# Optimization experiments

Hardware: AMD Instinct MI355X
Metric: run time of the kernel (lower is better)

The kernel has to match this reference:

```python
import jax, jax.numpy as jnp
import numpy as np

B, I, O, G = 4096, 256, 256, 8
GRID_MIN, GRID_MAX, RHO = -2.0, 2.0, 1.0


def setup_inputs() -> dict:
    key = jax.random.key(0)
    ks = jax.random.split(key, 8)
    return {
        "x_re": jax.random.normal(ks[0], (B, I), dtype=jnp.float32),
        "x_im": jax.random.normal(ks[1], (B, I), dtype=jnp.float32),
        "realweights": jax.random.normal(ks[2], (I, O, G, G), dtype=jnp.float32),
        "complexweights": jax.random.normal(ks[3], (I, O, G, G), dtype=jnp.float32),
        "silu_weight_re": jax.random.normal(ks[4], (I, O), dtype=jnp.float32),
        "silu_weight_im": jax.random.normal(ks[5], (I, O), dtype=jnp.float32),
        "silu_bias_re": 0.1 * jax.random.normal(ks[6], (I, O), dtype=jnp.float32),
        "silu_bias_im": 0.1 * jax.random.normal(ks[7], (I, O), dtype=jnp.float32),
    }


def reference(x_re, x_im, realweights, complexweights,
              silu_weight_re, silu_weight_im, silu_bias_re, silu_bias_im):
    # Complex grid: grid[u, v] = lin[u] + i * lin[v]
    lin = jnp.linspace(GRID_MIN, GRID_MAX, G, dtype=x_re.dtype)
    # |x - grid|^2 = (x_re - lin_u)^2 + (x_im - lin_v)^2  -> (B, I, G, G)
    dre = x_re[:, :, None, None] - lin[None, None, :, None]
    dim = x_im[:, :, None, None] - lin[None, None, None, :]
    basis = jnp.exp(-(dre * dre + dim * dim) / RHO)  # real-valued (B, I, G, G)
    # RBF contraction: real and imaginary output channels
    out_re = jnp.einsum('biuv,iouv->bo', basis, realweights)
    out_im = jnp.einsum('biuv,iouv->bo', basis, complexweights)
    # Complex SiLU (complex_weight variant): silu applied component-wise,
    # then complex-multiplied by silu_weight, plus bias, summed over i.
    s_re = jax.nn.silu(x_re)  # (B, I)
    s_im = jax.nn.silu(x_im)
    out_re = out_re + s_re @ silu_weight_re - s_im @ silu_weight_im + jnp.sum(silu_bias_re, axis=0)
    out_im = out_im + s_im @ silu_weight_re + s_re @ silu_weight_im + jnp.sum(silu_bias_im, axis=0)
    # Return complex output as stacked (real, imag): (B, O, 2)
    return jnp.stack([out_re, out_im], axis=-1)
```

## Files before the change

kernel.cpp:

```cpp
#include <hip/hip_runtime.h>
#include <hip/hip_fp16.h>
#include <stdint.h>

typedef float floatx4 __attribute__((ext_vector_type(4)));
typedef short short8 __attribute__((ext_vector_type(8)));

constexpr int I_SZ = 256, O_SZ = 256, NCOL = 512, B_SZ = 4096;
constexpr int KSTEPS = 264;
constexpr float GSTEP = 4.0f / 7.0f;
constexpr float NLOG2E = -1.44269504088896f;

__device__ __forceinline__ uint32_t pk_bf16(float lo, float hi) {
  return __builtin_amdgcn_perm(__float_as_uint(hi), __float_as_uint(lo), 0x07060302u);
}
__device__ __forceinline__ short rne_bf16(float f) {
  uint32_t u = __float_as_uint(f);
  return (short)((u + 0x7FFFu + ((u >> 16) & 1u)) >> 16);
}

__device__ __forceinline__ void gload_lds16(const void* g, void* l) {
  __builtin_amdgcn_global_load_lds((const __attribute__((address_space(1))) void*)g,
                                   (__attribute__((address_space(3))) void*)l,
                                   16, 0, 0);
}

__device__ __forceinline__ float silu_f(float a) {
  return a * __builtin_amdgcn_rcpf(1.f + __builtin_amdgcn_exp2f(a * NLOG2E));
}

__global__ void pack_weights(const float* __restrict__ rw, const float* __restrict__ cw,
                             const float* __restrict__ swre, const float* __restrict__ swim,
                             short* __restrict__ wpack) {
  int idx = blockIdx.x * 256 + threadIdx.x;
  int n = idx & 511;
  int slot = (idx >> 9) & 3;
  int ph = (idx >> 11) & 1;
  int s = idx >> 12;
  int u = ph * 4 + slot;
  int o = n >> 1, c = n & 1;
  float w[8];
  if (s < 256) {
    const float* W = (c ? cw : rw) + (((size_t)s * O_SZ + o) << 6) + (u << 3);
    float4 a = *(const float4*)W;
    float4 b = *(const float4*)(W + 4);
    w[0] = a.x; w[1] = a.y; w[2] = a.z; w[3] = a.w;
    w[4] = b.x; w[5] = b.y; w[6] = b.z; w[7] = b.w;
  } else {
    int kp0 = ((s - 256) << 6) + (u << 3);
    #pragma unroll
    for (int e = 0; e < 8; ++e) {
      int kp = kp0 + e, i = kp >> 1, ci = kp & 1;
      float a = swre[i * O_SZ + o], b = swim[i * O_SZ + o];
      w[e] = (c == 0) ? (ci == 0 ? a : -b) : (ci == 0 ? b : a);
    }
  }
  uint32_t h[8];
  #pragma unroll
  for (int e = 0; e < 8; ++e) h[e] = (uint32_t)(uint16_t)rne_bf16(w[e]);
  uint4 val = make_uint4(h[0] | (h[1] << 16), h[2] | (h[3] << 16),
                         h[4] | (h[5] << 16), h[6] | (h[7] << 16));
  *(uint4*)(wpack + (size_t)idx * 8) = val;
}

__global__ void transpose_x(const float* __restrict__ xre, const float* __restrict__ xim,
                            __half* __restrict__ xT) {
  __shared__ float tile[64][65];
  int bt = blockIdx.x & 63;
  int it = (blockIdx.x >> 6) & 3;
  int c  = blockIdx.x >> 8;
  const float* src = (c ? xim : xre);
  int b0 = bt << 6, i0 = it << 6;
  int t = threadIdx.x;
  int il = t & 63, bh = t >> 6;
  #pragma unroll
  for (int k = 0; k < 16; ++k) {
    int bl = bh + (k << 2);
    tile[bl][il] = src[(size_t)(b0 + bl) * I_SZ + i0 + il];
  }
  __syncthreads();
  int bl2 = t & 63, ih = t >> 6;
  __half* dst = xT + ((size_t)c * I_SZ + i0) * B_SZ + b0;
  #pragma unroll
  for (int k = 0; k < 16; ++k) {
    int il2 = ih + (k << 2);
    dst[(size_t)il2 * B_SZ + bl2] = __float2half(tile[bl2][il2]);
  }
}

__global__ void bias_sums(const float* __restrict__ bre, const float* __restrict__ bim,
                          float* __restrict__ bsum) {
  int n = blockIdx.x, o = n >> 1, l = threadIdx.x;
  const float* src = ((n & 1) ? bim : bre) + o;
  float s = 0.f;
  #pragma unroll
  for (int a = 0; a < 4; ++a) s += src[(size_t)(a * 64 + l) * O_SZ];
  #pragma unroll
  for (int off = 32; off; off >>= 1) s += __shfl_down(s, off, 64);
  if (l == 0) bsum[n] = s;
}

__global__ __launch_bounds__(512, 4) void cvkan_gemm(
    const float* __restrict__ xre, const float* __restrict__ xim,
    const __half* __restrict__ xT,
    const short* __restrict__ wpack, const float* __restrict__ bsum,
    float* __restrict__ out) {
  __shared__ __align__(16) short As[4 * 128 * 8];
  __shared__ __align__(16) short Bs[2][4 * 256 * 8];

  const int tid = threadIdx.x;
  const int bid = blockIdx.x;
  const int kch = bid & 7;
  const int mn = bid >> 3;
  const int mt = mn >> 1, nt = mn & 1;
  const int b0 = mt * 128, n0 = nt * 256;
  const int l = tid & 63, w = tid >> 6;
  const int wr = w >> 2, wc = w & 3;
  const int lm = l & 15, q = l >> 4;
  const int ar = tid & 127, au = tid >> 7;

  const __half* xTre = xT;
  const __half* xTim = xT + (size_t)I_SZ * B_SZ;

  floatx4 acc[4][4] = {};
  uint4 rA;
  float eiv[8];
  float xr_s;

  auto stage_B = [&](short* bdst, int t) {
    int js = t >> 1, ph = t & 1;
    int s = (js < 32) ? (kch * 32 + js) : (256 + kch);
    const short* src = wpack + (size_t)(s * 2 + ph) * 16384 + ((tid >> 8) << 12)
                       + (n0 << 3) + ((tid & 255) << 3);
    short* ldst = bdst + (w << 9);
    gload_lds16(src,        ldst);
    gload_lds16(src + 8192, ldst + 4096);
  };

  auto build_rbf = [&](int u, float xr) {
    float d = xr - (-2.0f + u * GSTEP);
    float er = __builtin_amdgcn_exp2f(d * d * NLOG2E);
    rA = make_uint4(pk_bf16(er * eiv[0], er * eiv[1]), pk_bf16(er * eiv[2], er * eiv[3]),
                    pk_bf16(er * eiv[4], er * eiv[5]), pk_bf16(er * eiv[6], er * eiv[7]));
  };

  auto build_silu = [&](int s, int u) {
    int sl = s - 256;
    const float* pr = xre + (size_t)(b0 + ar) * I_SZ + (sl << 5) + (u << 2);
    const float* pi = xim + (size_t)(b0 + ar) * I_SZ + (sl << 5) + (u << 2);
    rA = make_uint4(pk_bf16(silu_f(pr[0]), silu_f(pi[0])),
                    pk_bf16(silu_f(pr[1]), silu_f(pi[1])),
                    pk_bf16(silu_f(pr[2]), silu_f(pi[2])),
                    pk_bf16(silu_f(pr[3]), silu_f(pi[3])));
  };

  stage_B(&Bs[0][0], 0);
  {
    int s0 = kch * 32;
    float xi0 = __half2float(xTim[(size_t)s0 * B_SZ + b0 + ar]);
    xr_s = __half2float(xTre[(size_t)s0 * B_SZ + b0 + ar]);
    #pragma unroll
    for (int v = 0; v < 8; ++v) {
      float d = xi0 - (-2.0f + v * GSTEP);
      eiv[v] = __builtin_amdgcn_exp2f(d * d * NLOG2E);
    }
    build_rbf(au, xr_s);
  }

  short* bc = &Bs[0][0];
  short* bn = &Bs[1][0];
  float xr_n = 0.f, xi_n = 0.f;

  for (int t = 0; t < 66; ++t) {
    if (t < 65 && (t & 1) == 1) {
      int jsn = (t + 1) >> 1;
      if (jsn < 32) {
        int sn = kch * 32 + jsn;
        xr_n = __half2float(xTre[(size_t)sn * B_SZ + b0 + ar]);
        xi_n = __half2float(xTim[(size_t)sn * B_SZ + b0 + ar]);
      }
    }
    __builtin_amdgcn_sched_barrier(0);

    if (t < 65) stage_B(bn, t + 1);
    *(uint4*)(As + (au << 10) + (ar << 3)) = rA;

    if (t < 65) asm volatile("s_waitcnt vmcnt(2) lgkmcnt(0)" ::: "memory");
    else        asm volatile("s_waitcnt vmcnt(0) lgkmcnt(0)" ::: "memory");
    __builtin_amdgcn_s_barrier();

    if (t < 65) {
      int tn = t + 1, jsn = tn >> 1, phn = tn & 1;
      int sn = (jsn < 32) ? (kch * 32 + jsn) : (256 + kch);
      if (sn >= 256) {
        build_silu(sn, phn * 4 + au);
      } else if (phn == 0) {
        xr_s = xr_n;
        #pragma unroll
        for (int v = 0; v < 8; ++v) {
          float d = xi_n - (-2.0f + v * GSTEP);
          eiv[v] = __builtin_amdgcn_exp2f(d * d * NLOG2E);
        }
        build_rbf(au, xr_s);
      } else {
        build_rbf(4 + au, xr_s);
      }
    }

    short8 bf[4];
    #pragma unroll
    for (int nn = 0; nn < 4; ++nn)
      bf[nn] = *(const short8*)(bc + (q << 11) + ((wc * 64 + nn * 16 + lm) << 3));
    __builtin_amdgcn_s_setprio(1);
    #pragma unroll
    for (int mm = 0; mm < 4; ++mm) {
      short8 a = *(const short8*)(As + (q << 10) + ((wr * 64 + mm * 16 + lm) << 3));
      #pragma unroll
      for (int nn = 0; nn < 4; ++nn)
        acc[mm][nn] = __builtin_amdgcn_mfma_f32_16x16x32_bf16(a, bf[nn], acc[mm][nn], 0, 0, 0);
    }
    __builtin_amdgcn_s_setprio(0);

    if (t < 65) __builtin_amdgcn_s_barrier();
    short* tmp = bc; bc = bn; bn = tmp;
  }

  #pragma unroll
  for (int nn = 0; nn < 4; ++nn) {
    int col = n0 + wc * 64 + nn * 16 + lm;
    float bv = (kch == 7) ? bsum[col] : 0.0f;
    #pragma unroll
    for (int mm = 0; mm < 4; ++mm) {
      int row0 = b0 + wr * 64 + mm * 16 + (q << 2);
      #pragma unroll
      for (int r2 = 0; r2 < 4; ++r2)
        atomicAdd(out + (size_t)(row0 + r2) * NCOL + col, acc[mm][nn][r2] + bv);
    }
  }
}

extern "C" void kernel_launch(void* const* d_in, const int* in_sizes, int n_in,
                              void* d_out, int out_size, void* d_ws, size_t ws_size,
                              hipStream_t stream) {
  const float* xre  = (const float*)d_in[0];
  const float* xim  = (const float*)d_in[1];
  const float* rw   = (const float*)d_in[2];
  const float* cw   = (const float*)d_in[3];
  const float* swre = (const float*)d_in[4];
  const float* swim = (const float*)d_in[5];
  const float* bre  = (const float*)d_in[6];
  const float* bim  = (const float*)d_in[7];
  float* out = (float*)d_out;

  size_t wpack_bytes = (size_t)KSTEPS * NCOL * 64 * 2;
  short* wpack = (short*)d_ws;
  float* bsum  = (float*)((char*)d_ws + wpack_bytes);
  __half* xT   = (__half*)((char*)d_ws + wpack_bytes + 2048);

  hipMemsetAsync(d_out, 0, (size_t)B_SZ * NCOL * sizeof(float), stream);
  pack_weights<<<(KSTEPS * NCOL * 8) / 256, 256, 0, stream>>>(rw, cw, swre, swim, wpack);
  transpose_x<<<512, 256, 0, stream>>>(xre, xim, xT);
  bias_sums<<<NCOL, 64, 0, stream>>>(bre, bim, bsum);
  cvkan_gemm<<<512, 512, 0, stream>>>(xre, xim, xT, wpack, bsum, out);
}
```

Baseline: 232.5 us.

## Shrink GEMM tile to 128x128 with 256-thread blocks and restructure pipeline

Changes the fused RBF/SiLU GEMM from 128x256 tiles with 512 threads to 128x128 tiles with 256 threads and 1024 blocks. Each thread now builds two A-slices, recomputing the imaginary exponentials every step instead of caching them across phases. The pipeline is reworked so A is built after compute, between two full barriers, with a full vmcnt(0) wait. The aim is more blocks in flight and smaller LDS per block. The cost is more redundant RBF exp work, since each A tile is now built for twice as many N-tiles, plus extra barriers and a weaker load/compute overlap.

```diff
diff --git a/kernel.cpp b/kernel.cpp
--- a/kernel.cpp
+++ b/kernel.cpp
@@ -26,6 +26,12 @@
 
 __device__ __forceinline__ float silu_f(float a) {
   return a * __builtin_amdgcn_rcpf(1.f + __builtin_amdgcn_exp2f(a * NLOG2E));
+}
+
+__device__ __forceinline__ float h2f_raw(unsigned short u) {
+  _Float16 h;
+  __builtin_memcpy(&h, &u, 2);
+  return (float)h;
 }
 
 __global__ void pack_weights(const float* __restrict__ rw, const float* __restrict__ cw,
@@ -99,129 +105,126 @@
   if (l == 0) bsum[n] = s;
 }
 
-__global__ __launch_bounds__(512, 4) void cvkan_gemm(
+__global__ __launch_bounds__(256, 4) void cvkan_gemm(
     const float* __restrict__ xre, const float* __restrict__ xim,
     const __half* __restrict__ xT,
     const short* __restrict__ wpack, const float* __restrict__ bsum,
     float* __restrict__ out) {
   __shared__ __align__(16) short As[4 * 128 * 8];
-  __shared__ __align__(16) short Bs[2][4 * 256 * 8];
+  __shared__ __align__(16) short Bs[2][4 * 128 * 8];
 
   const int tid = threadIdx.x;
   const int bid = blockIdx.x;
   const int kch = bid & 7;
   const int mn = bid >> 3;
-  const int mt = mn >> 1, nt = mn & 1;
-  const int b0 = mt * 128, n0 = nt * 256;
+  const int mt = mn >> 2, nt = mn & 3;
+  const int b0 = mt * 128, n0 = nt * 128;
   const int l = tid & 63, w = tid >> 6;
-  const int wr = w >> 2, wc = w & 3;
+  const int wr = w >> 1, wc = w & 1;
   const int lm = l & 15, q = l >> 4;
-  const int ar = tid & 127, au = tid >> 7;
+  const int r = tid >> 1, h = tid & 1;
 
   const __half* xTre = xT;
   const __half* xTim = xT + (size_t)I_SZ * B_SZ;
 
   floatx4 acc[4][4] = {};
-  uint4 rA;
-  float eiv[8];
-  float xr_s;
 
   auto stage_B = [&](short* bdst, int t) {
     int js = t >> 1, ph = t & 1;
     int s = (js < 32) ? (kch * 32 + js) : (256 + kch);
-    const short* src = wpack + (size_t)(s * 2 + ph) * 16384 + ((tid >> 8) << 12)
-                       + (n0 << 3) + ((tid & 255) << 3);
+    const short* src = wpack + (size_t)s * 32768 + (size_t)ph * 16384
+                       + ((tid >> 7) << 12) + ((size_t)(n0 + (tid & 127)) << 3);
     short* ldst = bdst + (w << 9);
     gload_lds16(src,        ldst);
-    gload_lds16(src + 8192, ldst + 4096);
+    gload_lds16(src + 8192, ldst + 2048);
   };
 
-  auto build_rbf = [&](int u, float xr) {
-    float d = xr - (-2.0f + u * GSTEP);
-    float er = __builtin_amdgcn_exp2f(d * d * NLOG2E);
-    rA = make_uint4(pk_bf16(er * eiv[0], er * eiv[1]), pk_bf16(er * eiv[2], er * eiv[3]),
-                    pk_bf16(er * eiv[4], er * eiv[5]), pk_bf16(er * eiv[6], er * eiv[7]));
+  auto build_rbf = [&](int phn, float xr, float xi) {
+    float eiv[8];
+    #pragma unroll
+    for (int v = 0; v < 8; ++v) {
+      float d = xi - (-2.0f + v * GSTEP);
+      eiv[v] = __builtin_amdgcn_exp2f(d * d * NLOG2E);
+    }
+    #pragma unroll
+    for (int j = 0; j < 2; ++j) {
+      int u_loc = h * 2 + j;
+      int u = phn * 4 + u_loc;
+      float d = xr - (-2.0f + u * GSTEP);
+      float er = __builtin_amdgcn_exp2f(d * d * NLOG2E);
+      uint4 val = make_uint4(pk_bf16(er * eiv[0], er * eiv[1]), pk_bf16(er * eiv[2], er * eiv[3]),
+                             pk_bf16(er * eiv[4], er * eiv[5]), pk_bf16(er * eiv[6], er * eiv[7]));
+      *(uint4*)(As + u_loc * 1024 + r * 8) = val;
+    }
   };
 
-  auto build_silu = [&](int s, int u) {
-    int sl = s - 256;
-    const float* pr = xre + (size_t)(b0 + ar) * I_SZ + (sl << 5) + (u << 2);
-    const float* pi = xim + (size_t)(b0 + ar) * I_SZ + (sl << 5) + (u << 2);
-    rA = make_uint4(pk_bf16(silu_f(pr[0]), silu_f(pi[0])),
-                    pk_bf16(silu_f(pr[1]), silu_f(pi[1])),
-                    pk_bf16(silu_f(pr[2]), silu_f(pi[2])),
-                    pk_bf16(silu_f(pr[3]), silu_f(pi[3])));
+  auto build_silu = [&](int phn) {
+    #pragma unroll
+    for (int j = 0; j < 2; ++j) {
+      int u_loc = h * 2 + j;
+      int u = phn * 4 + u_loc;
+      const float* pr = xre + (size_t)(b0 + r) * I_SZ + (kch << 5) + (u << 2);
+      const float* pi = xim + (size_t)(b0 + r) * I_SZ + (kch << 5) + (u << 2);
+      uint4 val = make_uint4(pk_bf16(silu_f(pr[0]), silu_f(pi[0])),
+                             pk_bf16(silu_f(pr[1]), silu_f(pi[1])),
+                             pk_bf16(silu_f(pr[2]), silu_f(pi[2])),
+                             pk_bf16(silu_f(pr[3]), silu_f(pi[3])));
+      *(uint4*)(As + u_loc * 1024 + r * 8) = val;
+    }
   };
 
-  stage_B(&Bs[0][0], 0);
+  float xr_s, xi_s;
   {
     int s0 = kch * 32;
-    float xi0 = __half2float(xTim[(size_t)s0 * B_SZ + b0 + ar]);
-    xr_s = __half2float(xTre[(size_t)s0 * B_SZ + b0 + ar]);
-    #pragma unroll
-    for (int v = 0; v < 8; ++v) {
-      float d = xi0 - (-2.0f + v * GSTEP);
-      eiv[v] = __builtin_amdgcn_exp2f(d * d * NLOG2E);
-    }
-    build_rbf(au, xr_s);
-  }
-
-  short* bc = &Bs[0][0];
-  short* bn = &Bs[1][0];
-  float xr_n = 0.f, xi_n = 0.f;
+    xr_s = __half2float(xTre[(size_t)s0 * B_SZ + b0 + r]);
+    xi_s = __half2float(xTim[(size_t)s0 * B_SZ + b0 + r]);
+    stage_B(&Bs[0][0], 0);
+    build_rbf(0, xr_s, xi_s);
+    asm volatile("s_waitcnt vmcnt(0) lgkmcnt(0)" ::: "memory");
+  }
+  __syncthreads();
+
+  unsigned short hxr_n = 0, hxi_n = 0;
 
   for (int t = 0; t < 66; ++t) {
-    if (t < 65 && (t & 1) == 1) {
-      int jsn = (t + 1) >> 1;
-      if (jsn < 32) {
-        int sn = kch * 32 + jsn;
-        xr_n = __half2float(xTre[(size_t)sn * B_SZ + b0 + ar]);
-        xi_n = __half2float(xTim[(size_t)sn * B_SZ + b0 + ar]);
+    if (t < 65 && (t & 1)) {
+      int jn = (t + 1) >> 1;
+      if (jn < 32) {
+        int sn = kch * 32 + jn;
+        hxr_n = *(const unsigned short*)&xTre[(size_t)sn * B_SZ + b0 + r];
+        hxi_n = *(const unsigned short*)&xTim[(size_t)sn * B_SZ + b0 + r];
       }
     }
+    if (t < 65) stage_B(&Bs[(t + 1) & 1][0], t + 1);
     __builtin_amdgcn_sched_barrier(0);
 
-    if (t < 65) stage_B(bn, t + 1);
-    *(uint4*)(As + (au << 10) + (ar << 3)) = rA;
-
-    if (t < 65) asm volatile("s_waitcnt vmcnt(2) lgkmcnt(0)" ::: "memory");
-    else        asm volatile("s_waitcnt vmcnt(0) lgkmcnt(0)" ::: "memory");
-    __builtin_amdgcn_s_barrier();
-
-    if (t < 65) {
-      int tn = t + 1, jsn = tn >> 1, phn = tn & 1;
-      int sn = (jsn < 32) ? (kch * 32 + jsn) : (256 + kch);
-      if (sn >= 256) {
-        build_silu(sn, phn * 4 + au);
-      } else if (phn == 0) {
-        xr_s = xr_n;
-        #pragma unroll
-        for (int v = 0; v < 8; ++v) {
-          float d = xi_n - (-2.0f + v * GSTEP);
-          eiv[v] = __builtin_amdgcn_exp2f(d * d * NLOG2E);
-        }
-        build_rbf(au, xr_s);
-      } else {
-        build_rbf(4 + au, xr_s);
-      }
-    }
-
+    const short* bb = &Bs[t & 1][0];
     short8 bf[4];
     #pragma unroll
     for (int nn = 0; nn < 4; ++nn)
-      bf[nn] = *(const short8*)(bc + (q << 11) + ((wc * 64 + nn * 16 + lm) << 3));
+      bf[nn] = *(const short8*)(bb + q * 1024 + (wc * 64 + nn * 16 + lm) * 8);
     __builtin_amdgcn_s_setprio(1);
     #pragma unroll
     for (int mm = 0; mm < 4; ++mm) {
-      short8 a = *(const short8*)(As + (q << 10) + ((wr * 64 + mm * 16 + lm) << 3));
+      short8 a = *(const short8*)(As + q * 1024 + (wr * 64 + mm * 16 + lm) * 8);
       #pragma unroll
       for (int nn = 0; nn < 4; ++nn)
         acc[mm][nn] = __builtin_amdgcn_mfma_f32_16x16x32_bf16(a, bf[nn], acc[mm][nn], 0, 0, 0);
     }
     __builtin_amdgcn_s_setprio(0);
 
-    if (t < 65) __builtin_amdgcn_s_barrier();
-    short* tmp = bc; bc = bn; bn = tmp;
+    if (t < 65) {
+      __syncthreads();
+      int tn = t + 1, jn = tn >> 1, phn = tn & 1;
+      if (jn >= 32) {
+        build_silu(phn);
+      } else {
+        if (phn == 0) { xr_s = h2f_raw(hxr_n); xi_s = h2f_raw(hxi_n); }
+        build_rbf(phn, xr_s, xi_s);
+      }
+      asm volatile("s_waitcnt vmcnt(0) lgkmcnt(0)" ::: "memory");
+      __syncthreads();
+    }
   }
 
   #pragma unroll
@@ -260,5 +263,5 @@
   pack_weights<<<(KSTEPS * NCOL * 8) / 256, 256, 0, stream>>>(rw, cw, swre, swim, wpack);
   transpose_x<<<512, 256, 0, stream>>>(xre, xim, xT);
   bias_sums<<<NCOL, 64, 0, stream>>>(bre, bim, bsum);
-  cvkan_gemm<<<512, 512, 0, stream>>>(xre, xim, xT, wpack, bsum, out);
-}
+  cvkan_gemm<<<1024, 256, 0, stream>>>(xre, xim, xT, wpack, bsum, out);
+}
```

After: 242.2 us. 1.04x slower.
